# Optimization experiments

Measured on AMD Instinct MI355X. Metric: run time of the kernel, lower is better.

## Reference

```python
import jax, jax.numpy as jnp
import numpy as np
import math

N_HEADS = 16
D_HEAD = 64
D_MODEL = 1024
ROPE_THETA = 10000.0


def setup_inputs() -> dict:
    key = jax.random.key(0)
    k1, k2, k3 = jax.random.split(key, 3)
    B, T = 2, 2048
    x = jax.random.normal(k1, (B, T, D_MODEL), dtype=jnp.float32)
    # torch Linear(in, out) weight has shape (out, in); store transposed (in, out)
    # so forward is x @ w. Scale like default init to keep activations sane.
    w_qkv = jax.random.normal(k2, (D_MODEL, 3 * D_MODEL), dtype=jnp.float32) / math.sqrt(D_MODEL)
    w_o = jax.random.normal(k3, (D_MODEL, D_MODEL), dtype=jnp.float32) / math.sqrt(D_MODEL)
    return {"x": x, "w_qkv": w_qkv, "w_o": w_o}


def _build_rope(T, dtype):
    inv_freq = 1.0 / (ROPE_THETA ** (jnp.arange(0, D_HEAD, 2, dtype=jnp.float32) / D_HEAD))
    t = jnp.arange(T, dtype=jnp.float32)
    freqs = jnp.outer(t, inv_freq)            # [T, D_HEAD/2]
    emb = jnp.concatenate([freqs, freqs], -1)  # [T, D_HEAD]
    return jnp.cos(emb).astype(dtype), jnp.sin(emb).astype(dtype)


def _apply_rope(x, cos, sin):
    # x: [B, T, H, D_HEAD]; cos/sin broadcast as [1, T, 1, D_HEAD]
    x1, x2 = jnp.split(x, 2, axis=-1)
    rotated = jnp.concatenate([-x2, x1], axis=-1)
    return x * cos + rotated * sin


def reference(x, w_qkv, w_o):
    B, T, D = x.shape
    qkv = (x @ w_qkv).reshape(B, T, 3, N_HEADS, D_HEAD)
    q, k, v = qkv[:, :, 0], qkv[:, :, 1], qkv[:, :, 2]  # [B, T, H, Dh]
    cos, sin = _build_rope(T, x.dtype)
    cos = cos[None, :, None, :]
    sin = sin[None, :, None, :]
    q = _apply_rope(q, cos, sin)
    k = _apply_rope(k, cos, sin)
    scale = 1.0 / math.sqrt(D_HEAD)
    # full [B, H, T, T] scores (faithful to the manual matmul-softmax-matmul)
    attn = jnp.einsum("bthd,bshd->bhts", q, k) * scale
    attn = jax.nn.softmax(attn, axis=-1)
    out = jnp.einsum("bhts,bshd->bthd", attn, v).reshape(B, T, D)
    return out @ w_o
```

## Files before the change

### kernel.cpp

```cpp
#include <hip/hip_runtime.h>
#include <cstdint>

typedef unsigned short ushort_t;
typedef __attribute__((ext_vector_type(8))) short v8s;
typedef __attribute__((ext_vector_type(4))) short v4s;
typedef __attribute__((ext_vector_type(2))) unsigned v2u;
typedef __attribute__((ext_vector_type(4))) float v4f;

#define MFMA(a, b, c) __builtin_amdgcn_mfma_f32_16x16x32_bf16(a, b, c, 0, 0, 0)
#define QSCALE 0.18033688011112042f

__device__ __forceinline__ float bf2f(ushort_t u) {
    union { unsigned u; float f; } x; x.u = ((unsigned)u) << 16; return x.f;
}
__device__ __forceinline__ short f2bf(float f) {
    union { float f; unsigned u; } x; x.f = f;
    unsigned r = x.u + 0x7fffu + ((x.u >> 16) & 1u);
    return (short)(r >> 16);
}

__global__ void detect_dtype(const unsigned* __restrict__ x, int* __restrict__ flag) {
    __shared__ int cnt;
    if (threadIdx.x == 0) cnt = 0;
    __syncthreads();
    unsigned w = x[threadIdx.x];
    int e = (w >> 7) & 0xFF;
    int hit = ((e >= 96 && e <= 135) || (w & 0xFFFFu) == 0) ? 1 : 0;
    atomicAdd(&cnt, hit);
    __syncthreads();
    if (threadIdx.x == 0) *flag = (cnt >= 160) ? 1 : 0;
}

__global__ __launch_bounds__(256) void cvt_x(const void* __restrict__ xin,
                                             ushort_t* __restrict__ xb,
                                             const int* __restrict__ flagp, int n8) {
    int i = blockIdx.x * 256 + threadIdx.x;
    if (i >= n8) return;
    if (*flagp) {
        ((v8s*)xb)[i] = ((const v8s*)xin)[i];
    } else {
        const float* xf = (const float*)xin + (size_t)i * 8;
        v8s o;
        #pragma unroll
        for (int j = 0; j < 8; ++j) o[j] = f2bf(xf[j]);
        ((v8s*)xb)[i] = o;
    }
}

__global__ __launch_bounds__(256) void cvt_transpose(const void* __restrict__ in,
                                                     ushort_t* __restrict__ out,
                                                     const int* __restrict__ flagp,
                                                     int R, int C) {
    __shared__ ushort_t tile[32][33];
    int bx = blockIdx.x * 32, by = blockIdx.y * 32;
    int tx = threadIdx.x, ty = threadIdx.y;
    int isbf = *flagp;
    for (int i = ty; i < 32; i += 8) {
        size_t idx = (size_t)(by + i) * C + bx + tx;
        tile[i][tx] = isbf ? ((const ushort_t*)in)[idx]
                           : (ushort_t)f2bf(((const float*)in)[idx]);
    }
    __syncthreads();
    for (int i = ty; i < 32; i += 8) out[(size_t)(bx + i) * R + by + tx] = tile[tx][i];
}

__global__ __launch_bounds__(256) void rope_table(float* __restrict__ tab) {
    int idx = blockIdx.x * 256 + threadIdx.x;
    int t = idx >> 5, d = idx & 31;
    float inv_freq = __expf(-(float)d * 0.28782313662425575f);
    float ang = (float)t * inv_freq;
    float sn, cs;
    sincosf(ang, &sn, &cs);
    tab[t * 64 + d]      = bf2f((ushort_t)f2bf(cs));
    tab[t * 64 + 32 + d] = bf2f((ushort_t)f2bf(sn));
}

template <int MODE>
__global__ __launch_bounds__(256) void gemm_bt(const ushort_t* __restrict__ A,
                                               const ushort_t* __restrict__ BT,
                                               void* __restrict__ C,
                                               const int* __restrict__ flagp,
                                               int M, int N, int K,
                                               ushort_t* __restrict__ Qp,
                                               ushort_t* __restrict__ Kp,
                                               ushort_t* __restrict__ Vp,
                                               const float* __restrict__ tab) {
    __shared__ __align__(16) ushort_t As[128 * 32];
    __shared__ __align__(16) ushort_t Bs[128 * 32];
    int tid = threadIdx.x;
    int lane = tid & 63;
    int lr = lane & 15, lc = lane >> 4;
    int w = tid >> 6;
    int wr = (w >> 1) * 64, wc = (w & 1) * 64;
    int m0 = blockIdx.y * 128, n0 = blockIdx.x * 128;

    int c0 = tid, c1 = tid + 256;
    int r0 = c0 >> 2, s0 = c0 & 3;
    int r1 = c1 >> 2, s1 = c1 & 3;

    v4f acc[4][4] = {};

    for (int kt = 0; kt < K; kt += 32) {
        v8s a0 = *(const v8s*)(A + (size_t)(m0 + r0) * K + kt + s0 * 8);
        v8s a1 = *(const v8s*)(A + (size_t)(m0 + r1) * K + kt + s1 * 8);
        v8s b0 = *(const v8s*)(BT + (size_t)(n0 + r0) * K + kt + s0 * 8);
        v8s b1 = *(const v8s*)(BT + (size_t)(n0 + r1) * K + kt + s1 * 8);
        __syncthreads();
        *(v8s*)(As + (size_t)c0 * 8) = a0;
        *(v8s*)(As + (size_t)c1 * 8) = a1;
        *(v8s*)(Bs + (size_t)c0 * 8) = b0;
        *(v8s*)(Bs + (size_t)c1 * 8) = b1;
        __syncthreads();

        v8s af[4], bfr[4];
        #pragma unroll
        for (int i = 0; i < 4; ++i)
            af[i] = *(const v8s*)(As + (wr + i * 16 + lr) * 32 + lc * 8);
        #pragma unroll
        for (int j = 0; j < 4; ++j)
            bfr[j] = *(const v8s*)(Bs + (wc + j * 16 + lr) * 32 + lc * 8);
        #pragma unroll
        for (int i = 0; i < 4; ++i)
            #pragma unroll
            for (int j = 0; j < 4; ++j)
                acc[i][j] = MFMA(af[i], bfr[j], acc[i][j]);
    }

    if (MODE == 1) {
        int store_f32 = (*flagp == 0);
        #pragma unroll
        for (int i = 0; i < 4; ++i)
            #pragma unroll
            for (int j = 0; j < 4; ++j)
                #pragma unroll
                for (int r = 0; r < 4; ++r) {
                    int row = m0 + wr + i * 16 + lc * 4 + r;
                    int col = n0 + wc + j * 16 + lr;
                    if (store_f32)
                        ((float*)C)[(size_t)row * N + col] = acc[i][j][r];
                    else
                        ((ushort_t*)C)[(size_t)row * N + col] = (ushort_t)f2bf(acc[i][j][r]);
                }
    } else {
        int region = n0 >> 10;
        int h = ((n0 & 1023) + wc) >> 6;
        if (region < 2) {
            const float sc = (region == 0) ? QSCALE : 1.0f;
            ushort_t* dst = (region == 0) ? Qp : Kp;
            #pragma unroll
            for (int i = 0; i < 4; ++i)
                #pragma unroll
                for (int j = 0; j < 2; ++j) {
                    int d = j * 16 + lr;
                    #pragma unroll
                    for (int r = 0; r < 4; ++r) {
                        int tg = m0 + wr + i * 16 + lc * 4 + r;
                        int b = tg >> 11, tt = tg & 2047;
                        float cs = tab[tt * 64 + d], sn = tab[tt * 64 + 32 + d];
                        float x1 = acc[i][j][r], x2 = acc[i][j + 2][r];
                        size_t base = ((size_t)(b * 16 + h) * 2048 + tt) * 64 + d;
                        dst[base]      = (ushort_t)f2bf((x1 * cs - x2 * sn) * sc);
                        dst[base + 32] = (ushort_t)f2bf((x2 * cs + x1 * sn) * sc);
                    }
                }
        } else {
            #pragma unroll
            for (int i = 0; i < 4; ++i)
                #pragma unroll
                for (int j = 0; j < 4; ++j) {
                    int d = j * 16 + lr;
                    int tg0 = m0 + wr + i * 16 + lc * 4;
                    int b = tg0 >> 11, tt = tg0 & 2047;
                    v4s pk;
                    #pragma unroll
                    for (int r = 0; r < 4; ++r) pk[r] = f2bf(acc[i][j][r]);
                    size_t base = (size_t)(b * 16 + h) * 131072 + (size_t)(tt >> 5) * 2048
                                + (size_t)d * 32 + (tt & 31);
                    *(v4s*)(Vp + base) = pk;
                }
        }
    }
}

__global__ __launch_bounds__(256) void attn(const ushort_t* __restrict__ Qr,
                                            const ushort_t* __restrict__ Kr,
                                            const ushort_t* __restrict__ Vt,
                                            ushort_t* __restrict__ AO) {
    __shared__ __align__(16) ushort_t Ks[2][2048];
    __shared__ __align__(16) ushort_t Vs[2][2048];
    __shared__ __align__(16) ushort_t P[4][2560];
    int tid = threadIdx.x, lane = tid & 63, W = tid >> 6;
    int lr = lane & 15, lc = lane >> 4;
    int L = blockIdx.x;
    int bh = (L & 7) * 4 + ((L >> 3) & 3);
    int qt = L >> 5;
    int q0 = qt * 256 + W * 64;
    int b = bh >> 4, h = bh & 15;
    const ushort_t* Qb = Qr + ((size_t)bh * 2048 + q0) * 64;
    const ushort_t* Kb = Kr + (size_t)bh * 131072;
    const ushort_t* Vb = Vt + (size_t)bh * 131072;
    ushort_t* Pw = P[W];

    int krow = tid >> 3, kchk = tid & 7;
    const ushort_t* Kg = Kb + (size_t)krow * 64 + kchk * 8;
    int klds = krow * 64 + (kchk ^ (krow & 7)) * 8;
    const ushort_t* Vg = Vb + (size_t)tid * 8;
    int vlds = tid * 8;

    v8s qf[4][2];
    #pragma unroll
    for (int jq = 0; jq < 4; ++jq)
        #pragma unroll
        for (int kk = 0; kk < 2; ++kk)
            qf[jq][kk] = *(const v8s*)(Qb + (size_t)(jq * 16 + lr) * 64 + kk * 32 + lc * 8);

    v4f o[4][4] = {};
    float li[4] = {0.f, 0.f, 0.f, 0.f};

    v8s kreg = *(const v8s*)(Kg);
    v8s vreg = *(const v8s*)(Vg);
    *(v8s*)(&Ks[0][klds]) = kreg;
    *(v8s*)(&Vs[0][vlds]) = vreg;
    kreg = *(const v8s*)(Kg + 2048);
    vreg = *(const v8s*)(Vg + 2048);
    __syncthreads();

    #pragma unroll 1
    for (int t = 0; t < 64; ++t) {
        int p = t & 1;
        const ushort_t* Kl = Ks[p];
        const ushort_t* Vl = Vs[p];

        v8s kf[2][2], vf[4];
        #pragma unroll
        for (int hh = 0; hh < 2; ++hh)
            #pragma unroll
            for (int kk = 0; kk < 2; ++kk)
                kf[hh][kk] = *(const v8s*)(Kl + (hh * 16 + lr) * 64 + (((kk * 4 + lc) ^ (lr & 7)) * 8));
        #pragma unroll
        for (int i = 0; i < 4; ++i)
            vf[i] = *(const v8s*)(Vl + (i * 16 + lr) * 32 + lc * 8);

        v4f St[2][4] = {};
        #pragma unroll
        for (int hh = 0; hh < 2; ++hh)
            #pragma unroll
            for (int jq = 0; jq < 4; ++jq) {
                St[hh][jq] = MFMA(kf[hh][0], qf[jq][0], St[hh][jq]);
                St[hh][jq] = MFMA(kf[hh][1], qf[jq][1], St[hh][jq]);
            }

        if (t + 1 < 64) {
            *(v8s*)(&Ks[p ^ 1][klds]) = kreg;
            *(v8s*)(&Vs[p ^ 1][vlds]) = vreg;
        }
        if (t + 2 < 64) {
            kreg = *(const v8s*)(Kg + (size_t)(t + 2) * 2048);
            vreg = *(const v8s*)(Vg + (size_t)(t + 2) * 2048);
        }

        #pragma unroll
        for (int jq = 0; jq < 4; ++jq)
            #pragma unroll
            for (int hh = 0; hh < 2; ++hh) {
                #pragma unroll
                for (int r = 0; r < 4; ++r) {
                    float ev = __builtin_amdgcn_exp2f(St[hh][jq][r]);
                    St[hh][jq][r] = ev;
                    li[jq] += ev;
                }
                unsigned d0 = __builtin_amdgcn_perm(__float_as_uint(St[hh][jq][1]),
                                                    __float_as_uint(St[hh][jq][0]), 0x07060302u);
                unsigned d1 = __builtin_amdgcn_perm(__float_as_uint(St[hh][jq][3]),
                                                    __float_as_uint(St[hh][jq][2]), 0x07060302u);
                v2u pk = {d0, d1};
                *(v2u*)(Pw + (jq * 16 + lr) * 40 + hh * 16 + lc * 4) = pk;
            }
        __builtin_amdgcn_s_waitcnt(0xc07f);
        #pragma unroll
        for (int jq = 0; jq < 4; ++jq) {
            v8s pf = *(const v8s*)(Pw + (jq * 16 + lr) * 40 + lc * 8);
            #pragma unroll
            for (int i = 0; i < 4; ++i)
                o[i][jq] = MFMA(vf[i], pf, o[i][jq]);
        }
        __syncthreads();
    }

    #pragma unroll
    for (int jq = 0; jq < 4; ++jq) {
        li[jq] += __shfl_xor(li[jq], 16);
        li[jq] += __shfl_xor(li[jq], 32);
        float inv = 1.0f / li[jq];
        int t = q0 + jq * 16 + lr;
        #pragma unroll
        for (int i = 0; i < 4; ++i) {
            v4s pk;
            #pragma unroll
            for (int r = 0; r < 4; ++r) pk[r] = f2bf(o[i][jq][r] * inv);
            *(v4s*)(AO + (size_t)(b * 2048 + t) * 1024 + h * 64 + i * 16 + lc * 4) = pk;
        }
    }
}

extern "C" void kernel_launch(void* const* d_in, const int* in_sizes, int n_in,
                              void* d_out, int out_size, void* d_ws, size_t ws_size,
                              hipStream_t stream) {
    char* ws = (char*)d_ws;
    int*      flag  = (int*)ws;
    ushort_t* wqkvT = (ushort_t*)(ws + 256);
    ushort_t* woT   = (ushort_t*)(ws + 6291712);
    ushort_t* xb    = (ushort_t*)(ws + 8388864);
    ushort_t* Qr    = (ushort_t*)(ws + 16777472);
    ushort_t* Kr    = (ushort_t*)(ws + 25166080);
    ushort_t* Vt    = (ushort_t*)(ws + 33554688);
    ushort_t* AO    = (ushort_t*)(ws + 41943296);
    float*    tab   = (float*)(ws + 50331904);

    detect_dtype<<<1, 256, 0, stream>>>((const unsigned*)d_in[0], flag);
    rope_table<<<256, 256, 0, stream>>>(tab);
    cvt_x<<<2048, 256, 0, stream>>>(d_in[0], xb, flag, 524288);
    dim3 tb(32, 8);
    cvt_transpose<<<dim3(96, 32), tb, 0, stream>>>(d_in[1], wqkvT, flag, 1024, 3072);
    cvt_transpose<<<dim3(32, 32), tb, 0, stream>>>(d_in[2], woT, flag, 1024, 1024);
    gemm_bt<2><<<dim3(24, 32), 256, 0, stream>>>(xb, wqkvT, nullptr, flag, 4096, 3072, 1024,
                                                 Qr, Kr, Vt, tab);
    attn<<<256, 256, 0, stream>>>(Qr, Kr, Vt, AO);
    gemm_bt<1><<<dim3(8, 32), 256, 0, stream>>>(AO, woT, d_out, flag, 4096, 1024, 1024,
                                                nullptr, nullptr, nullptr, nullptr);
}
```

Before: 218.7 us.

## Split attention KV range across wave pairs and merge partial outputs in LDS

The attention kernel now gives each block 128 queries instead of 256 and launches 512 blocks. Two wave pairs each handle half of the 2048 keys, and the partial outputs and row sums are combined through LDS at the end. The aim is to double the block count and fill more of the MI355X CUs, since 256 blocks underfill the device. In exchange, each block does its own K/V loads for only half as many queries, LDS use grows to about 52KB, and an extra merge step with a sync is added. The merge relies on the softmax having no max subtraction, so partial exp-sums can simply be added.

```diff
diff --git a/kernel.cpp b/kernel.cpp
--- a/kernel.cpp
+++ b/kernel.cpp
@@ -186,26 +186,32 @@
                                             const ushort_t* __restrict__ Kr,
                                             const ushort_t* __restrict__ Vt,
                                             ushort_t* __restrict__ AO) {
-    __shared__ __align__(16) ushort_t Ks[2][2048];
-    __shared__ __align__(16) ushort_t Vs[2][2048];
-    __shared__ __align__(16) ushort_t P[4][2560];
+    __shared__ __align__(16) char lds[53248];
     int tid = threadIdx.x, lane = tid & 63, W = tid >> 6;
     int lr = lane & 15, lc = lane >> 4;
+    int qsub = W & 1, sh = W >> 1;
     int L = blockIdx.x;
     int bh = (L & 7) * 4 + ((L >> 3) & 3);
     int qt = L >> 5;
-    int q0 = qt * 256 + W * 64;
+    int q0 = qt * 128 + qsub * 64;
     int b = bh >> 4, h = bh & 15;
     const ushort_t* Qb = Qr + ((size_t)bh * 2048 + q0) * 64;
-    const ushort_t* Kb = Kr + (size_t)bh * 131072;
-    const ushort_t* Vb = Vt + (size_t)bh * 131072;
-    ushort_t* Pw = P[W];
-
-    int krow = tid >> 3, kchk = tid & 7;
-    const ushort_t* Kg = Kb + (size_t)krow * 64 + kchk * 8;
-    int klds = krow * 64 + (kchk ^ (krow & 7)) * 8;
-    const ushort_t* Vg = Vb + (size_t)tid * 8;
-    int vlds = tid * 8;
+    const ushort_t* Kb = Kr + (size_t)bh * 131072 + (size_t)sh * 65536;
+    const ushort_t* Vb = Vt + (size_t)bh * 131072 + (size_t)sh * 65536;
+    ushort_t* Pw  = (ushort_t*)(lds + 32768 + W * 5120);
+    ushort_t* KsG = (ushort_t*)(lds + sh * 16384);
+    ushort_t* VsG = (ushort_t*)(lds + sh * 16384 + 8192);
+
+    int gt = tid & 127;
+    int c0 = gt, c1 = gt + 128;
+    int kr0 = c0 >> 3, kc0 = c0 & 7, kr1 = c1 >> 3, kc1 = c1 & 7;
+    const ushort_t* Kg0 = Kb + (size_t)kr0 * 64 + kc0 * 8;
+    const ushort_t* Kg1 = Kb + (size_t)kr1 * 64 + kc1 * 8;
+    int kl0 = kr0 * 64 + (kc0 ^ (kr0 & 7)) * 8;
+    int kl1 = kr1 * 64 + (kc1 ^ (kr1 & 7)) * 8;
+    const ushort_t* Vg0 = Vb + (size_t)c0 * 8;
+    const ushort_t* Vg1 = Vb + (size_t)c1 * 8;
+    int vl0 = c0 * 8, vl1 = c1 * 8;
 
     v8s qf[4][2];
     #pragma unroll
@@ -217,19 +223,23 @@
     v4f o[4][4] = {};
     float li[4] = {0.f, 0.f, 0.f, 0.f};
 
-    v8s kreg = *(const v8s*)(Kg);
-    v8s vreg = *(const v8s*)(Vg);
-    *(v8s*)(&Ks[0][klds]) = kreg;
-    *(v8s*)(&Vs[0][vlds]) = vreg;
-    kreg = *(const v8s*)(Kg + 2048);
-    vreg = *(const v8s*)(Vg + 2048);
+    v8s ka = *(const v8s*)(Kg0), kb2 = *(const v8s*)(Kg1);
+    v8s va = *(const v8s*)(Vg0), vb2 = *(const v8s*)(Vg1);
+    *(v8s*)(KsG + kl0) = ka;
+    *(v8s*)(KsG + kl1) = kb2;
+    *(v8s*)(VsG + vl0) = va;
+    *(v8s*)(VsG + vl1) = vb2;
+    ka  = *(const v8s*)(Kg0 + 2048);
+    kb2 = *(const v8s*)(Kg1 + 2048);
+    va  = *(const v8s*)(Vg0 + 2048);
+    vb2 = *(const v8s*)(Vg1 + 2048);
     __syncthreads();
 
     #pragma unroll 1
-    for (int t = 0; t < 64; ++t) {
+    for (int t = 0; t < 32; ++t) {
         int p = t & 1;
-        const ushort_t* Kl = Ks[p];
-        const ushort_t* Vl = Vs[p];
+        const ushort_t* Kl = KsG + p * 2048;
+        const ushort_t* Vl = VsG + p * 2048;
 
         v8s kf[2][2], vf[4];
         #pragma unroll
@@ -250,13 +260,19 @@
                 St[hh][jq] = MFMA(kf[hh][1], qf[jq][1], St[hh][jq]);
             }
 
-        if (t + 1 < 64) {
-            *(v8s*)(&Ks[p ^ 1][klds]) = kreg;
-            *(v8s*)(&Vs[p ^ 1][vlds]) = vreg;
-        }
-        if (t + 2 < 64) {
-            kreg = *(const v8s*)(Kg + (size_t)(t + 2) * 2048);
-            vreg = *(const v8s*)(Vg + (size_t)(t + 2) * 2048);
+        if (t + 1 < 32) {
+            ushort_t* Kn = KsG + (p ^ 1) * 2048;
+            ushort_t* Vn = VsG + (p ^ 1) * 2048;
+            *(v8s*)(Kn + kl0) = ka;
+            *(v8s*)(Kn + kl1) = kb2;
+            *(v8s*)(Vn + vl0) = va;
+            *(v8s*)(Vn + vl1) = vb2;
+        }
+        if (t + 2 < 32) {
+            ka  = *(const v8s*)(Kg0 + (size_t)(t + 2) * 2048);
+            kb2 = *(const v8s*)(Kg1 + (size_t)(t + 2) * 2048);
+            va  = *(const v8s*)(Vg0 + (size_t)(t + 2) * 2048);
+            vb2 = *(const v8s*)(Vg1 + (size_t)(t + 2) * 2048);
         }
 
         #pragma unroll
@@ -291,14 +307,33 @@
     for (int jq = 0; jq < 4; ++jq) {
         li[jq] += __shfl_xor(li[jq], 16);
         li[jq] += __shfl_xor(li[jq], 32);
-        float inv = 1.0f / li[jq];
-        int t = q0 + jq * 16 + lr;
-        #pragma unroll
-        for (int i = 0; i < 4; ++i) {
-            v4s pk;
-            #pragma unroll
-            for (int r = 0; r < 4; ++r) pk[r] = f2bf(o[i][jq][r] * inv);
-            *(v4s*)(AO + (size_t)(b * 2048 + t) * 1024 + h * 64 + i * 16 + lc * 4) = pk;
+    }
+    float* MO = (float*)(lds + qsub * 17408);
+    float* Ml = (float*)(lds + 34816 + qsub * 256);
+    __syncthreads();
+    if (sh == 1) {
+        #pragma unroll
+        for (int jq = 0; jq < 4; ++jq) {
+            #pragma unroll
+            for (int i = 0; i < 4; ++i)
+                *(v4f*)(MO + (jq * 16 + lr) * 68 + i * 16 + lc * 4) = o[i][jq];
+            if (lc == 0) Ml[jq * 16 + lr] = li[jq];
+        }
+    }
+    __syncthreads();
+    if (sh == 0) {
+        #pragma unroll
+        for (int jq = 0; jq < 4; ++jq) {
+            float inv = 1.0f / (li[jq] + Ml[jq * 16 + lr]);
+            int t = q0 + jq * 16 + lr;
+            #pragma unroll
+            for (int i = 0; i < 4; ++i) {
+                v4f m = *(const v4f*)(MO + (jq * 16 + lr) * 68 + i * 16 + lc * 4);
+                v4s pk;
+                #pragma unroll
+                for (int r = 0; r < 4; ++r) pk[r] = f2bf((o[i][jq][r] + m[r]) * inv);
+                *(v4s*)(AO + (size_t)(b * 2048 + t) * 1024 + h * 64 + i * 16 + lc * 4) = pk;
+            }
         }
     }
 }
@@ -325,7 +360,7 @@
     cvt_transpose<<<dim3(32, 32), tb, 0, stream>>>(d_in[2], woT, flag, 1024, 1024);
     gemm_bt<2><<<dim3(24, 32), 256, 0, stream>>>(xb, wqkvT, nullptr, flag, 4096, 3072, 1024,
                                                  Qr, Kr, Vt, tab);
-    attn<<<256, 256, 0, stream>>>(Qr, Kr, Vt, AO);
+    attn<<<512, 256, 0, stream>>>(Qr, Kr, Vt, AO);
     gemm_bt<1><<<dim3(8, 32), 256, 0, stream>>>(AO, woT, d_out, flag, 4096, 1024, 1024,
                                                 nullptr, nullptr, nullptr, nullptr);
 }
```

New measurement: 211.7 us. -3.2%, faster.
